# Performance work log

Hardware: AMD Instinct MI355X
Metric: run time of the kernel (lower is better)

Reference implementation:

```python
import jax, jax.numpy as jnp
import numpy as np

NEG = -10000000.0

def setup_inputs() -> dict:
    key0 = jax.random.key(0)
    ks = jax.random.split(key0, 5)
    B, XL, KL, D = 16, 1024, 512, 1024  # D = 2*rnn_dim
    return {
        "x": jax.random.normal(ks[0], (B, XL, D), dtype=jnp.float32),
        "x_mask": jnp.ones((B, XL), dtype=jnp.float32),
        "key": jax.random.normal(ks[1], (B, KL, D), dtype=jnp.float32),
        "key_mask": jnp.ones((B, KL), dtype=jnp.float32),
        "w_input": jax.random.normal(ks[2], (D,), dtype=jnp.float32) / np.sqrt(D),
        "w_key": jax.random.normal(ks[3], (D,), dtype=jnp.float32) / np.sqrt(D),
        "dot_w": jax.random.normal(ks[4], (D,), dtype=jnp.float32) / np.sqrt(D),
    }

def reference(x, x_mask, key, key_mask, w_input, w_key, dot_w):
    # Trilinear attention score S[b,i,j] = w_in.x_i + w_key.k_j + (x_i*dot_w).k_j
    x_logits = jnp.einsum('bxd,d->bx', x, w_input)      # [B, XL]
    key_logits = jnp.einsum('bkd,d->bk', key, w_key)    # [B, KL]
    S = (x_logits[:, :, None] + key_logits[:, None, :]
         + jnp.einsum('bxd,bkd->bxk', x * dot_w, key))  # [B, XL, KL]

    # x -> key attention with joint mask
    joint_mask = 1.0 - x_mask[:, :, None] * key_mask[:, None, :]
    masked_S = S + joint_mask * NEG
    attn = jax.nn.softmax(masked_S, axis=-1)
    x2key = jnp.einsum('bxk,bkd->bxd', attn, key)       # [B, XL, D]

    # key -> x attention: mask over key dim, max-reduce, masked softmax over x
    km = key_mask[:, None, :]
    S2 = S * km + (1.0 - km) * NEG                      # add_masked_value
    max_s = jnp.max(S2, axis=-1)                        # [B, XL]
    p = jax.nn.softmax(max_s * x_mask, axis=-1) * x_mask  # claf masked_softmax
    p = p / (jnp.sum(p, axis=-1, keepdims=True) + 1e-13)
    key2x = jnp.einsum('bx,bxd->bd', p, x)[:, None, :]  # [B, 1, D], broadcasts

    key2x_full = jnp.broadcast_to(key2x, x.shape)
    return jnp.concatenate([x, x2key, x * x2key, x * key2x_full], axis=-1)
```

## Files before the change

### kernel.cpp

```cpp
#include <hip/hip_runtime.h>
#include <hip/hip_fp16.h>

#define B_ 16
#define XL_ 1024
#define KL_ 512
#define D_ 1024
#define NEGC (-10000000.0f)

typedef _Float16 f16x8 __attribute__((ext_vector_type(8)));
typedef float f32x4 __attribute__((ext_vector_type(4)));
typedef unsigned short u16x8 __attribute__((ext_vector_type(8)));
typedef unsigned short u16x4 __attribute__((ext_vector_type(4)));

__device__ __forceinline__ unsigned short f2h(float f) {
  __half h = __float2half(f);
  return __half_as_ushort(h);
}

__global__ __launch_bounds__(256) void k_build(const float* __restrict__ key,
    const float* __restrict__ w_key, unsigned short* __restrict__ KQ2,
    unsigned short* __restrict__ KV2, float* __restrict__ klog) {
  __shared__ unsigned short tile[64][72];
  int bid = blockIdx.x;
  int b = bid >> 4;
  int ks = (bid >> 1) & 7;
  int dh = bid & 1;
  int tid = threadIdx.x;
  int kr = tid >> 2;
  int cq = tid & 3;
  const float* krow = key + ((size_t)(b * KL_ + ks * 64 + kr)) * D_;
  float klacc = 0.f;
  int dl = tid & 63, g = tid >> 6;

  for (int dt = dh * 8; dt < dh * 8 + 8; ++dt) {
#pragma unroll
    for (int j = 0; j < 4; ++j) {
      int c = dt * 64 + cq * 16 + j * 4;
      float4 v = *(const float4*)(krow + c);
      float4 w = *(const float4*)(w_key + c);
      klacc += v.x * w.x + v.y * w.y + v.z * w.z + v.w * w.w;
      u16x4 hv;
      hv[0] = f2h(v.x); hv[1] = f2h(v.y); hv[2] = f2h(v.z); hv[3] = f2h(v.w);
      *(u16x4*)(&tile[kr][cq * 16 + j * 4]) = hv;
    }
    __syncthreads();
#pragma unroll
    for (int dkc_l = 0; dkc_l < 2; ++dkc_l) {
      u16x8 hv = *(const u16x8*)(&tile[kr][dkc_l * 32 + cq * 8]);
      size_t dst = (((size_t)(b * 8 + ks) * 32 + (dt * 2 + dkc_l)) << 11)
                   + (size_t)(((kr >> 4) & 3) * 512 + (cq * 16 + (kr & 15)) * 8);
      *(u16x8*)(KQ2 + dst) = hv;
    }
    {
      int dglob = dt * 64 + dl;
      int wv_ = dglob >> 7, np = (dglob >> 4) & 7, l15v = dglob & 15;
#pragma unroll
      for (int kkc_l = 0; kkc_l < 2; ++kkc_l) {
        u16x8 hv;
#pragma unroll
        for (int h = 0; h < 8; ++h) hv[h] = tile[kkc_l * 32 + g * 8 + h][dl];
        size_t dst = (((size_t)(b * 8 + wv_) * 16 + (ks * 2 + kkc_l)) << 12)
                     + (size_t)(np * 512 + (g * 16 + l15v) * 8);
        *(u16x8*)(KV2 + dst) = hv;
      }
    }
    __syncthreads();
  }
  klacc += __shfl_xor(klacc, 1);
  klacc += __shfl_xor(klacc, 2);
  if (cq == 0) atomicAdd(&klog[b * KL_ + ks * 64 + kr], klacc);
}

__global__ __launch_bounds__(512, 4) void k_attn(
    const float* __restrict__ x, const float* __restrict__ x_mask,
    const float* __restrict__ key_mask, const float* __restrict__ dot_w,
    const float* __restrict__ w_input,
    const unsigned short* __restrict__ KQ2, const unsigned short* __restrict__ KV2,
    const float* __restrict__ klog,
    float* __restrict__ maxs, float* __restrict__ out) {
  __shared__ unsigned short Qall[32 * 1024];
  __shared__ float xlg[32];
  unsigned short* Pt = Qall;
  float* redA = (float*)(Qall + 16384);
  float* redB = redA + 256;
  float* redC = redB + 256;

  const int tid = threadIdx.x;
  const int wv = tid >> 6;
  const int lane = tid & 63;
  const int l15 = lane & 15, l4 = lane >> 4;
  const int r7 = l15 & 7;

  int bid = blockIdx.x;
  int b = (bid & 7) * 2 + (bid >> 8);
  int x0 = ((bid >> 3) & 31) * 32;

  const float* xB = x + ((size_t)b * XL_ + x0) * D_;

  {
    int row = tid >> 4;
    int cg = tid & 15;
    const float* sp = xB + (size_t)row * D_;
    char* qrow = (char*)Qall + row * 2048;
    int rsw = row & 7;
    float xl = 0.f;
#pragma unroll
    for (int j = 0; j < 16; ++j) {
      int c4 = cg + j * 16;
      float4 v = *(const float4*)(sp + c4 * 4);
      float4 w = *(const float4*)(dot_w + c4 * 4);
      float4 wi = *(const float4*)(w_input + c4 * 4);
      xl += v.x * wi.x + v.y * wi.y + v.z * wi.z + v.w * wi.w;
      u16x4 hv;
      hv[0] = f2h(v.x * w.x); hv[1] = f2h(v.y * w.y);
      hv[2] = f2h(v.z * w.z); hv[3] = f2h(v.w * w.w);
      *(u16x4*)(qrow + (((c4 >> 1) ^ rsw) << 4) + ((c4 & 1) << 3)) = hv;
    }
    xl += __shfl_xor(xl, 1);
    xl += __shfl_xor(xl, 2);
    xl += __shfl_xor(xl, 4);
    xl += __shfl_xor(xl, 8);
    if (cg == 0) xlg[row] = xl;
  }
  __syncthreads();

  f32x4 acc[2][4];
#pragma unroll
  for (int m = 0; m < 2; ++m)
#pragma unroll
    for (int n = 0; n < 4; ++n) { f32x4 z = {0.f, 0.f, 0.f, 0.f}; acc[m][n] = z; }

  const unsigned short* KQ2w = KQ2 + (((size_t)(b * 8 + wv) * 32) << 11) + lane * 8;
  const char* qa0 = (char*)Qall + l15 * 2048;
  const char* qa1 = (char*)Qall + (16 + l15) * 2048;

#pragma unroll 4
  for (int dk = 0; dk < D_; dk += 32) {
    const unsigned short* cp = KQ2w + ((dk >> 5) << 11);
    f16x8 b0 = *(const f16x8*)(cp);
    f16x8 b1 = *(const f16x8*)(cp + 512);
    f16x8 b2 = *(const f16x8*)(cp + 1024);
    f16x8 b3 = *(const f16x8*)(cp + 1536);
    int c = (((dk >> 3) + l4) ^ r7) << 4;
    f16x8 a0 = *(const f16x8*)(qa0 + c);
    f16x8 a1 = *(const f16x8*)(qa1 + c);
    __builtin_amdgcn_s_setprio(1);
    acc[0][0] = __builtin_amdgcn_mfma_f32_16x16x32_f16(b0, a0, acc[0][0], 0, 0, 0);
    acc[1][0] = __builtin_amdgcn_mfma_f32_16x16x32_f16(b0, a1, acc[1][0], 0, 0, 0);
    acc[0][1] = __builtin_amdgcn_mfma_f32_16x16x32_f16(b1, a0, acc[0][1], 0, 0, 0);
    acc[1][1] = __builtin_amdgcn_mfma_f32_16x16x32_f16(b1, a1, acc[1][1], 0, 0, 0);
    acc[0][2] = __builtin_amdgcn_mfma_f32_16x16x32_f16(b2, a0, acc[0][2], 0, 0, 0);
    acc[1][2] = __builtin_amdgcn_mfma_f32_16x16x32_f16(b2, a1, acc[1][2], 0, 0, 0);
    acc[0][3] = __builtin_amdgcn_mfma_f32_16x16x32_f16(b3, a0, acc[0][3], 0, 0, 0);
    acc[1][3] = __builtin_amdgcn_mfma_f32_16x16x32_f16(b3, a1, acc[1][3], 0, 0, 0);
    __builtin_amdgcn_s_setprio(0);
  }
  __syncthreads();

  float xlv[2], xmv[2];
#pragma unroll
  for (int m = 0; m < 2; ++m) {
    int row = m * 16 + l15;
    xlv[m] = xlg[row];
    xmv[m] = x_mask[(size_t)b * XL_ + x0 + row];
  }
  f32x4 klv[4], kmv[4];
#pragma unroll
  for (int n = 0; n < 4; ++n) {
    int kb = wv * 64 + n * 16 + l4 * 4;
    klv[n] = *(const f32x4*)(klog + (size_t)b * KL_ + kb);
    kmv[n] = *(const f32x4*)(key_mask + (size_t)b * KL_ + kb);
  }
  float mxsm[2] = {-3.0e38f, -3.0e38f}, mxs2[2] = {-3.0e38f, -3.0e38f};
#pragma unroll
  for (int m = 0; m < 2; ++m)
#pragma unroll
    for (int n = 0; n < 4; ++n)
#pragma unroll
      for (int q = 0; q < 4; ++q) {
        float s = acc[m][n][q] + xlv[m] + klv[n][q];
        float sm = s + (1.f - xmv[m] * kmv[n][q]) * NEGC;
        float s2 = s * kmv[n][q] + (1.f - kmv[n][q]) * NEGC;
        mxsm[m] = fmaxf(mxsm[m], sm);
        mxs2[m] = fmaxf(mxs2[m], s2);
      }
#pragma unroll
  for (int m = 0; m < 2; ++m) {
    mxsm[m] = fmaxf(mxsm[m], __shfl_xor(mxsm[m], 16));
    mxsm[m] = fmaxf(mxsm[m], __shfl_xor(mxsm[m], 32));
    mxs2[m] = fmaxf(mxs2[m], __shfl_xor(mxs2[m], 16));
    mxs2[m] = fmaxf(mxs2[m], __shfl_xor(mxs2[m], 32));
  }
  if (l4 == 0) {
#pragma unroll
    for (int m = 0; m < 2; ++m) {
      redA[wv * 32 + m * 16 + l15] = mxsm[m];
      redB[wv * 32 + m * 16 + l15] = mxs2[m];
    }
  }
  __syncthreads();
  float gmx[2];
#pragma unroll
  for (int m = 0; m < 2; ++m) {
    int row = m * 16 + l15;
    float v = redA[row];
#pragma unroll
    for (int w = 1; w < 8; ++w) v = fmaxf(v, redA[w * 32 + row]);
    gmx[m] = v;
  }
  if (tid < 32) {
    float v = redB[tid];
#pragma unroll
    for (int w = 1; w < 8; ++w) v = fmaxf(v, redB[w * 32 + tid]);
    maxs[(size_t)b * XL_ + x0 + tid] = v;
  }
  float rs[2] = {0.f, 0.f};
#pragma unroll
  for (int m = 0; m < 2; ++m) {
    int row = m * 16 + l15;
    char* prow = (char*)Pt + row * 1024;
    int rsw = row & 7;
#pragma unroll
    for (int n = 0; n < 4; ++n) {
      int k = wv * 64 + n * 16 + l4 * 4;
      u16x4 pk;
#pragma unroll
      for (int q = 0; q < 4; ++q) {
        float s = acc[m][n][q] + xlv[m] + klv[n][q];
        float sm = s + (1.f - xmv[m] * kmv[n][q]) * NEGC;
        float e = __expf(sm - gmx[m]);
        rs[m] += e;
        pk[q] = f2h(e);
      }
      *(u16x4*)(prow + ((((k >> 3) ^ rsw) << 4) + ((k & 4) << 1))) = pk;
    }
  }
#pragma unroll
  for (int m = 0; m < 2; ++m) {
    rs[m] += __shfl_xor(rs[m], 16);
    rs[m] += __shfl_xor(rs[m], 32);
  }
  if (l4 == 0) {
#pragma unroll
    for (int m = 0; m < 2; ++m) redC[wv * 32 + m * 16 + l15] = rs[m];
  }
  __syncthreads();

  float dn[2];
#pragma unroll
  for (int m = 0; m < 2; ++m) {
    int row = m * 16 + l15;
    float sum = redC[row];
#pragma unroll
    for (int w = 1; w < 8; ++w) sum += redC[w * 32 + row];
    dn[m] = 1.f / sum;
  }
  size_t obase0 = ((size_t)b * XL_ + x0) * (size_t)(4 * D_);
  const char* pa0 = (char*)Pt + l15 * 1024;
  const char* pa1 = (char*)Pt + (16 + l15) * 1024;
  const unsigned short* KV2w = KV2 + (((size_t)(b * 8 + wv) * 16) << 12) + lane * 8;
#pragma unroll
  for (int sc = 0; sc < 2; ++sc) {
    int c0 = wv * 128 + sc * 64;
    f32x4 acc2[2][4];
#pragma unroll
    for (int m = 0; m < 2; ++m)
#pragma unroll
      for (int n = 0; n < 4; ++n) { f32x4 z = {0.f, 0.f, 0.f, 0.f}; acc2[m][n] = z; }
    const unsigned short* KV2s = KV2w + sc * 4 * 512;
#pragma unroll 4
    for (int kk = 0; kk < KL_; kk += 32) {
      const unsigned short* cp = KV2s + ((kk >> 5) << 12);
      f16x8 b0 = *(const f16x8*)(cp);
      f16x8 b1 = *(const f16x8*)(cp + 512);
      f16x8 b2 = *(const f16x8*)(cp + 1024);
      f16x8 b3 = *(const f16x8*)(cp + 1536);
      int c = ((((kk >> 3) + l4) ^ r7) << 4);
      f16x8 a0 = *(const f16x8*)(pa0 + c);
      f16x8 a1 = *(const f16x8*)(pa1 + c);
      __builtin_amdgcn_s_setprio(1);
      acc2[0][0] = __builtin_amdgcn_mfma_f32_16x16x32_f16(b0, a0, acc2[0][0], 0, 0, 0);
      acc2[1][0] = __builtin_amdgcn_mfma_f32_16x16x32_f16(b0, a1, acc2[1][0], 0, 0, 0);
      acc2[0][1] = __builtin_amdgcn_mfma_f32_16x16x32_f16(b1, a0, acc2[0][1], 0, 0, 0);
      acc2[1][1] = __builtin_amdgcn_mfma_f32_16x16x32_f16(b1, a1, acc2[1][1], 0, 0, 0);
      acc2[0][2] = __builtin_amdgcn_mfma_f32_16x16x32_f16(b2, a0, acc2[0][2], 0, 0, 0);
      acc2[1][2] = __builtin_amdgcn_mfma_f32_16x16x32_f16(b2, a1, acc2[1][2], 0, 0, 0);
      acc2[0][3] = __builtin_amdgcn_mfma_f32_16x16x32_f16(b3, a0, acc2[0][3], 0, 0, 0);
      acc2[1][3] = __builtin_amdgcn_mfma_f32_16x16x32_f16(b3, a1, acc2[1][3], 0, 0, 0);
      __builtin_amdgcn_s_setprio(0);
    }
#pragma unroll
    for (int m = 0; m < 2; ++m) {
      int row = m * 16 + l15;
      size_t ob = obase0 + (size_t)row * (4 * D_);
      const float* xr = xB + (size_t)row * D_;
#pragma unroll
      for (int n = 0; n < 4; ++n) {
        int col = c0 + n * 16 + l4 * 4;
        f32x4 v = acc2[m][n];
        v[0] *= dn[m]; v[1] *= dn[m]; v[2] *= dn[m]; v[3] *= dn[m];
        f32x4 xv = *(const f32x4*)(xr + col);
        *(f32x4*)(out + ob + col) = xv;
        *(f32x4*)(out + ob + D_ + col) = v;
        f32x4 pv;
        pv[0] = v[0] * xv[0]; pv[1] = v[1] * xv[1];
        pv[2] = v[2] * xv[2]; pv[3] = v[3] * xv[3];
        *(f32x4*)(out + ob + 2 * D_ + col) = pv;
      }
    }
  }
}

__global__ __launch_bounds__(256) void k_p(const float* __restrict__ maxs,
    const float* __restrict__ x_mask, float* __restrict__ pbuf) {
  int b = blockIdx.x, tid = threadIdx.x;
  int wv = tid >> 6, lane = tid & 63;
  __shared__ float r1[4], r2[4], r3[4];
  const float* ms = maxs + (size_t)b * XL_;
  const float* xm = x_mask + (size_t)b * XL_;
  float tv[4], xmv[4];
  float vmax = -3.0e38f;
#pragma unroll
  for (int i = 0; i < 4; ++i) {
    int xi = i * 256 + tid;
    xmv[i] = xm[xi];
    tv[i] = ms[xi] * xmv[i];
    vmax = fmaxf(vmax, tv[i]);
  }
#pragma unroll
  for (int sh = 32; sh >= 1; sh >>= 1) vmax = fmaxf(vmax, __shfl_xor(vmax, sh));
  if (lane == 0) r1[wv] = vmax;
  __syncthreads();
  float gmax = fmaxf(fmaxf(r1[0], r1[1]), fmaxf(r1[2], r1[3]));
  float e[4]; float es = 0.f;
#pragma unroll
  for (int i = 0; i < 4; ++i) { e[i] = __expf(tv[i] - gmax); es += e[i]; }
#pragma unroll
  for (int sh = 32; sh >= 1; sh >>= 1) es += __shfl_xor(es, sh);
  if (lane == 0) r2[wv] = es;
  __syncthreads();
  float gsum = r2[0] + r2[1] + r2[2] + r2[3];
  float pv[4]; float ps = 0.f;
#pragma unroll
  for (int i = 0; i < 4; ++i) { pv[i] = e[i] / gsum * xmv[i]; ps += pv[i]; }
#pragma unroll
  for (int sh = 32; sh >= 1; sh >>= 1) ps += __shfl_xor(ps, sh);
  if (lane == 0) r3[wv] = ps;
  __syncthreads();
  float gps = r3[0] + r3[1] + r3[2] + r3[3];
  float inv = 1.f / (gps + 1e-13f);
#pragma unroll
  for (int i = 0; i < 4; ++i) pbuf[(size_t)b * XL_ + i * 256 + tid] = pv[i] * inv;
}

__global__ __launch_bounds__(256) void k_key2x_part(const float* __restrict__ x,
    const float* __restrict__ pbuf, float* __restrict__ partial) {
  int b = blockIdx.x >> 4;
  int xc = blockIdx.x & 15;
  __shared__ float ps[64];
  if (threadIdx.x < 64) ps[threadIdx.x] = pbuf[(size_t)b * XL_ + xc * 64 + threadIdx.x];
  __syncthreads();
  const float* xb = x + ((size_t)b * XL_ + xc * 64) * D_;
  float acc0 = 0.f, acc1 = 0.f, acc2 = 0.f, acc3 = 0.f;
  int d = threadIdx.x;
  for (int xi = 0; xi < 64; ++xi) {
    float pv = ps[xi];
    const float* rp = xb + (size_t)xi * D_;
    acc0 += pv * rp[d];
    acc1 += pv * rp[d + 256];
    acc2 += pv * rp[d + 512];
    acc3 += pv * rp[d + 768];
  }
  float* pp = partial + (size_t)blockIdx.x * D_;
  pp[d] = acc0; pp[d + 256] = acc1; pp[d + 512] = acc2; pp[d + 768] = acc3;
}

__global__ __launch_bounds__(256) void k_key2x_red(const float* __restrict__ partial,
    float* __restrict__ k2x) {
  int idx = blockIdx.x * 256 + threadIdx.x;
  int b = idx >> 10;
  float s = 0.f;
#pragma unroll
  for (int xc = 0; xc < 16; ++xc)
    s += partial[((size_t)b * 16 + xc) * D_ + (idx & 1023)];
  k2x[idx] = s;
}

__global__ __launch_bounds__(256) void k_outfinal(const float* __restrict__ x,
    const float* __restrict__ k2x, float* __restrict__ out) {
  size_t t = (size_t)blockIdx.x * 256 + threadIdx.x;
  size_t base = t * 4;
  int b = (int)(base >> 20);
  int rem = (int)(base & ((1u << 20) - 1));
  int xr = rem >> 10;
  int d = rem & 1023;
  float4 xv = *(const float4*)(x + base);
  float4 kv = *(const float4*)(k2x + (size_t)b * D_ + d);
  float* orow = out + ((size_t)b * XL_ + xr) * (size_t)(4 * D_);
  float4 pr;
  pr.x = xv.x * kv.x; pr.y = xv.y * kv.y; pr.z = xv.z * kv.z; pr.w = xv.w * kv.w;
  *(float4*)(orow + 3 * D_ + d) = pr;
}

extern "C" void kernel_launch(void* const* d_in, const int* in_sizes, int n_in,
                              void* d_out, int out_size, void* d_ws, size_t ws_size,
                              hipStream_t stream) {
  (void)in_sizes; (void)n_in; (void)out_size; (void)ws_size;
  const float* x        = (const float*)d_in[0];
  const float* x_mask   = (const float*)d_in[1];
  const float* key      = (const float*)d_in[2];
  const float* key_mask = (const float*)d_in[3];
  const float* w_input  = (const float*)d_in[4];
  const float* w_key    = (const float*)d_in[5];
  const float* dot_w    = (const float*)d_in[6];
  float* out = (float*)d_out;
  char* ws = (char*)d_ws;

  unsigned short* KQ2 = (unsigned short*)ws;
  unsigned short* KV2 = (unsigned short*)(ws + (16u << 20));
  float* xlog = (float*)(ws + (32u << 20));
  float* klog = xlog + B_ * XL_;
  float* maxs = klog + B_ * KL_;
  float* pbuf = maxs + B_ * XL_;
  float* k2x  = pbuf + B_ * XL_;
  float* partial = (float*)ws;

  hipMemsetAsync(klog, 0, B_ * KL_ * sizeof(float), stream);
  k_build<<<dim3(B_ * 16), dim3(256), 0, stream>>>(key, w_key, KQ2, KV2, klog);
  k_attn<<<dim3(512), dim3(512), 0, stream>>>(x, x_mask, key_mask, dot_w, w_input,
                                              KQ2, KV2, klog, maxs, out);
  k_p<<<dim3(B_), dim3(256), 0, stream>>>(maxs, x_mask, pbuf);
  k_key2x_part<<<dim3(B_ * 16), dim3(256), 0, stream>>>(x, pbuf, partial);
  k_key2x_red<<<dim3(B_ * D_ / 256), dim3(256), 0, stream>>>(partial, k2x);
  k_outfinal<<<dim3(B_ * XL_ * D_ / 1024), dim3(256), 0, stream>>>(x, k2x, out);
}
```

Measured before the change: 165.9 us.

## Fuse softmax into key2x partial kernel and use nontemporal stores/loads

The small k_p softmax kernel is folded into k_key2x_part, so each block recomputes the per-batch softmax weights redundantly and one launch is dropped. The copy of x into the first output slice moves from the epilogue to the prologue, where x is already loaded, which avoids rereading it. Output writes and streaming reads of x switch to nontemporal loads and stores to reduce cache pollution. The cost is redundant softmax work across 16 blocks per batch, plus possible cache effects on x, which is read again in later kernels.

```diff
diff --git a/kernel.cpp b/kernel.cpp
--- a/kernel.cpp
+++ b/kernel.cpp
@@ -101,19 +101,21 @@
     int row = tid >> 4;
     int cg = tid & 15;
     const float* sp = xB + (size_t)row * D_;
+    float* outx = out + ((size_t)b * XL_ + x0 + row) * (size_t)(4 * D_);
     char* qrow = (char*)Qall + row * 2048;
     int rsw = row & 7;
     float xl = 0.f;
 #pragma unroll
     for (int j = 0; j < 16; ++j) {
       int c4 = cg + j * 16;
-      float4 v = *(const float4*)(sp + c4 * 4);
-      float4 w = *(const float4*)(dot_w + c4 * 4);
-      float4 wi = *(const float4*)(w_input + c4 * 4);
-      xl += v.x * wi.x + v.y * wi.y + v.z * wi.z + v.w * wi.w;
+      f32x4 v = *(const f32x4*)(sp + c4 * 4);
+      f32x4 w = *(const f32x4*)(dot_w + c4 * 4);
+      f32x4 wi = *(const f32x4*)(w_input + c4 * 4);
+      xl += v[0] * wi[0] + v[1] * wi[1] + v[2] * wi[2] + v[3] * wi[3];
+      __builtin_nontemporal_store(v, (f32x4*)(outx + c4 * 4));
       u16x4 hv;
-      hv[0] = f2h(v.x * w.x); hv[1] = f2h(v.y * w.y);
-      hv[2] = f2h(v.z * w.z); hv[3] = f2h(v.w * w.w);
+      hv[0] = f2h(v[0] * w[0]); hv[1] = f2h(v[1] * w[1]);
+      hv[2] = f2h(v[2] * w[2]); hv[3] = f2h(v[3] * w[3]);
       *(u16x4*)(qrow + (((c4 >> 1) ^ rsw) << 4) + ((c4 & 1) << 3)) = hv;
     }
     xl += __shfl_xor(xl, 1);
@@ -300,22 +302,25 @@
         f32x4 v = acc2[m][n];
         v[0] *= dn[m]; v[1] *= dn[m]; v[2] *= dn[m]; v[3] *= dn[m];
         f32x4 xv = *(const f32x4*)(xr + col);
-        *(f32x4*)(out + ob + col) = xv;
-        *(f32x4*)(out + ob + D_ + col) = v;
+        __builtin_nontemporal_store(v, (f32x4*)(out + ob + D_ + col));
         f32x4 pv;
         pv[0] = v[0] * xv[0]; pv[1] = v[1] * xv[1];
         pv[2] = v[2] * xv[2]; pv[3] = v[3] * xv[3];
-        *(f32x4*)(out + ob + 2 * D_ + col) = pv;
+        __builtin_nontemporal_store(pv, (f32x4*)(out + ob + 2 * D_ + col));
       }
     }
   }
 }
 
-__global__ __launch_bounds__(256) void k_p(const float* __restrict__ maxs,
-    const float* __restrict__ x_mask, float* __restrict__ pbuf) {
-  int b = blockIdx.x, tid = threadIdx.x;
-  int wv = tid >> 6, lane = tid & 63;
+__global__ __launch_bounds__(256) void k_key2x_part(const float* __restrict__ x,
+    const float* __restrict__ maxs, const float* __restrict__ x_mask,
+    float* __restrict__ partial) {
+  int b = blockIdx.x >> 4;
+  int xc = blockIdx.x & 15;
+  int tid = threadIdx.x;
+  int wvi = tid >> 6, lane = tid & 63;
   __shared__ float r1[4], r2[4], r3[4];
+  __shared__ float ps_all[XL_];
   const float* ms = maxs + (size_t)b * XL_;
   const float* xm = x_mask + (size_t)b * XL_;
   float tv[4], xmv[4];
@@ -329,7 +334,7 @@
   }
 #pragma unroll
   for (int sh = 32; sh >= 1; sh >>= 1) vmax = fmaxf(vmax, __shfl_xor(vmax, sh));
-  if (lane == 0) r1[wv] = vmax;
+  if (lane == 0) r1[wvi] = vmax;
   __syncthreads();
   float gmax = fmaxf(fmaxf(r1[0], r1[1]), fmaxf(r1[2], r1[3]));
   float e[4]; float es = 0.f;
@@ -337,39 +342,32 @@
   for (int i = 0; i < 4; ++i) { e[i] = __expf(tv[i] - gmax); es += e[i]; }
 #pragma unroll
   for (int sh = 32; sh >= 1; sh >>= 1) es += __shfl_xor(es, sh);
-  if (lane == 0) r2[wv] = es;
+  if (lane == 0) r2[wvi] = es;
   __syncthreads();
   float gsum = r2[0] + r2[1] + r2[2] + r2[3];
-  float pv[4]; float ps = 0.f;
-#pragma unroll
-  for (int i = 0; i < 4; ++i) { pv[i] = e[i] / gsum * xmv[i]; ps += pv[i]; }
-#pragma unroll
-  for (int sh = 32; sh >= 1; sh >>= 1) ps += __shfl_xor(ps, sh);
-  if (lane == 0) r3[wv] = ps;
+  float pv4[4]; float psum = 0.f;
+#pragma unroll
+  for (int i = 0; i < 4; ++i) { pv4[i] = e[i] / gsum * xmv[i]; psum += pv4[i]; }
+#pragma unroll
+  for (int sh = 32; sh >= 1; sh >>= 1) psum += __shfl_xor(psum, sh);
+  if (lane == 0) r3[wvi] = psum;
   __syncthreads();
   float gps = r3[0] + r3[1] + r3[2] + r3[3];
   float inv = 1.f / (gps + 1e-13f);
 #pragma unroll
-  for (int i = 0; i < 4; ++i) pbuf[(size_t)b * XL_ + i * 256 + tid] = pv[i] * inv;
-}
-
-__global__ __launch_bounds__(256) void k_key2x_part(const float* __restrict__ x,
-    const float* __restrict__ pbuf, float* __restrict__ partial) {
-  int b = blockIdx.x >> 4;
-  int xc = blockIdx.x & 15;
-  __shared__ float ps[64];
-  if (threadIdx.x < 64) ps[threadIdx.x] = pbuf[(size_t)b * XL_ + xc * 64 + threadIdx.x];
+  for (int i = 0; i < 4; ++i) ps_all[i * 256 + tid] = pv4[i] * inv;
   __syncthreads();
   const float* xb = x + ((size_t)b * XL_ + xc * 64) * D_;
   float acc0 = 0.f, acc1 = 0.f, acc2 = 0.f, acc3 = 0.f;
-  int d = threadIdx.x;
+  int d = tid;
+  const float* psl = ps_all + xc * 64;
   for (int xi = 0; xi < 64; ++xi) {
-    float pv = ps[xi];
+    float pv = psl[xi];
     const float* rp = xb + (size_t)xi * D_;
-    acc0 += pv * rp[d];
-    acc1 += pv * rp[d + 256];
-    acc2 += pv * rp[d + 512];
-    acc3 += pv * rp[d + 768];
+    acc0 += pv * __builtin_nontemporal_load(rp + d);
+    acc1 += pv * __builtin_nontemporal_load(rp + d + 256);
+    acc2 += pv * __builtin_nontemporal_load(rp + d + 512);
+    acc3 += pv * __builtin_nontemporal_load(rp + d + 768);
   }
   float* pp = partial + (size_t)blockIdx.x * D_;
   pp[d] = acc0; pp[d + 256] = acc1; pp[d + 512] = acc2; pp[d + 768] = acc3;
@@ -394,12 +392,13 @@
   int rem = (int)(base & ((1u << 20) - 1));
   int xr = rem >> 10;
   int d = rem & 1023;
-  float4 xv = *(const float4*)(x + base);
-  float4 kv = *(const float4*)(k2x + (size_t)b * D_ + d);
+  f32x4 xv = __builtin_nontemporal_load((const f32x4*)(x + base));
+  f32x4 kv = *(const f32x4*)(k2x + (size_t)b * D_ + d);
   float* orow = out + ((size_t)b * XL_ + xr) * (size_t)(4 * D_);
-  float4 pr;
-  pr.x = xv.x * kv.x; pr.y = xv.y * kv.y; pr.z = xv.z * kv.z; pr.w = xv.w * kv.w;
-  *(float4*)(orow + 3 * D_ + d) = pr;
+  f32x4 pr;
+  pr[0] = xv[0] * kv[0]; pr[1] = xv[1] * kv[1];
+  pr[2] = xv[2] * kv[2]; pr[3] = xv[3] * kv[3];
+  __builtin_nontemporal_store(pr, (f32x4*)(orow + 3 * D_ + d));
 }
 
 extern "C" void kernel_launch(void* const* d_in, const int* in_sizes, int n_in,
@@ -429,8 +428,7 @@
   k_build<<<dim3(B_ * 16), dim3(256), 0, stream>>>(key, w_key, KQ2, KV2, klog);
   k_attn<<<dim3(512), dim3(512), 0, stream>>>(x, x_mask, key_mask, dot_w, w_input,
                                               KQ2, KV2, klog, maxs, out);
-  k_p<<<dim3(B_), dim3(256), 0, stream>>>(maxs, x_mask, pbuf);
-  k_key2x_part<<<dim3(B_ * 16), dim3(256), 0, stream>>>(x, pbuf, partial);
+  k_key2x_part<<<dim3(B_ * 16), dim3(256), 0, stream>>>(x, maxs, x_mask, partial);
   k_key2x_red<<<dim3(B_ * D_ / 256), dim3(256), 0, stream>>>(partial, k2x);
   k_outfinal<<<dim3(B_ * XL_ * D_ / 1024), dim3(256), 0, stream>>>(x, k2x, out);
 }
```

New measurement: 172.8 us. 4.2% more time.
